# Kernel optimization log

Hardware: AMD Instinct MI355X
Metric: run time of the kernel (lower is better)

## Reference

```python
import jax, jax.numpy as jnp
import numpy as np

B, F_DIM, T = 16, 256, 4096
L = 128           # latent_dim
CF = 2            # combineVQ_frames
K = 2             # codebook_num
M = 1024          # codebook_size (n_embeddings)
D = L * CF // K   # codebook_dim = 128
TC = T // CF      # combined frames
ALPHA = -5.0      # distance->logit scale
TAU = 2.0         # max_temp (curr_temp at init)


def setup_inputs() -> dict:
    key = jax.random.key(0)
    k1, k2, k3, k4, k5 = jax.random.split(key, 5)
    inputs = jax.random.normal(k1, (B, F_DIM, T, 1), dtype=jnp.float32)
    # xavier-ish scaled 1x1 conv weights
    w1 = jax.random.normal(k2, (L, F_DIM), dtype=jnp.float32) * (2.0 / (L + F_DIM)) ** 0.5
    w2 = jax.random.normal(k3, (F_DIM, L), dtype=jnp.float32) * (2.0 / (L + F_DIM)) ** 0.5
    # codebooks init uniform(-1, 1) as in nn.init.uniform_(a=-1, b=1)
    codebooks = jax.random.uniform(k4, (K, M, D), dtype=jnp.float32, minval=-1.0, maxval=1.0)
    # gumbel noise that torch's F.gumbel_softmax would sample internally
    u = jax.random.uniform(k5, (K, B * TC, M), dtype=jnp.float32, minval=1e-7, maxval=1.0 - 1e-7)
    gumbels = -jnp.log(-jnp.log(u))
    return {"inputs": inputs, "w1": w1, "w2": w2, "codebooks": codebooks, "gumbels": gumbels}


def _vq_layer(vq_in, emb, g):
    # vq_in: [B, TC, D], emb: [M, D], g: [B*TC, M]
    xf = vq_in.reshape(-1, D)  # [N, D]
    dist = (jnp.sum(emb ** 2, axis=1)[None, :]
            + jnp.sum(xf ** 2, axis=1, keepdims=True)
            - 2.0 * (xf @ emb.T))                      # [N, M]
    logits = ALPHA * dist
    # straight-through hard gumbel-softmax (training path of F.gumbel_softmax(hard=True))
    y_soft = jax.nn.softmax((logits + g) / TAU, axis=-1)
    idx = jnp.argmax(y_soft, axis=-1)                  # [N]
    y_hard = jax.nn.one_hot(idx, M, dtype=y_soft.dtype)
    y = y_hard + y_soft - jax.lax.stop_gradient(y_soft)
    q = y @ emb                                        # [N, D] dequantize
    return q.reshape(B, TC, D), idx.reshape(B, TC)


def reference(inputs, w1, w2, codebooks, gumbels):
    # conv1x1_1: [B, F, T, 1] -> [B, L, T, 1]; then squeeze(-1).permute(0,2,1) -> [B, T, L]
    x = jnp.einsum('bfto,lf->btl', inputs, w1)         # [B, T, L]
    # combine frames and split channels across codebooks
    xc = x.reshape(B, TC, CF, L)                       # [B, TC, CF, L]
    chunks = jnp.split(xc, K, axis=-1)                 # K x [B, TC, CF, L/K]
    quants, inds = [], []
    for i in range(K):
        vq_in = chunks[i].reshape(B, TC, D)            # CF*(L/K) == D
        q, idx = _vq_layer(vq_in, codebooks[i], gumbels[i])
        quants.append(q.reshape(B, TC, CF, L // K))
        inds.append(idx)
    vq_feat = jnp.concatenate(quants, axis=-1).reshape(B, T, L)  # [B, T, L]
    # conv1x1_2: back to [B, F, T, 1]
    out = jnp.einsum('btl,fl->bft', vq_feat, w2)[..., None]
    quant_inds = jnp.stack(inds, axis=-1)              # [B, TC, K]
    return out, vq_feat, quant_inds
```

## Files before the change

kernel.cpp:

```cpp
#include <hip/hip_runtime.h>
#include <cstdint>
#include <cmath>

#define B_ 16
#define F_ 256
#define T_ 4096
#define L_ 128
#define TC_ 2048
#define D_ 128
#define M_ 1024
#define NROWS_ 32768

#define PAD 132

__global__ __launch_bounds__(256) void gemm1_kernel(
    const float* __restrict__ in, const float* __restrict__ w1,
    float* __restrict__ x) {
  __shared__ float As[32 * PAD];
  __shared__ float Bs[32 * PAD];
  const int tid = threadIdx.x;
  const int blk = blockIdx.x;
  const int b = blk >> 5;
  const int t0 = (blk & 31) << 7;
  const int tm = tid & 15;
  const int tr = tid >> 4;
  const float* inb = in + (size_t)b * F_ * T_;
  float acc[8][8];
#pragma unroll
  for (int i = 0; i < 8; ++i)
#pragma unroll
    for (int j = 0; j < 8; ++j) acc[i][j] = 0.f;

  for (int f0 = 0; f0 < F_; f0 += 32) {
#pragma unroll
    for (int it = 0; it < 4; ++it) {
      int e = tid + it * 256;
      int ff = e >> 5, q = e & 31;
      float4 v = *(const float4*)(inb + (size_t)(f0 + ff) * T_ + t0 + q * 4);
      *(float4*)(&As[ff * PAD + q * 4]) = v;
    }
#pragma unroll
    for (int it = 0; it < 4; ++it) {
      int e = tid + it * 256;
      int l = e >> 3, q = e & 7;
      float4 v = *(const float4*)(w1 + l * F_ + f0 + q * 4);
      Bs[(q * 4 + 0) * PAD + l] = v.x;
      Bs[(q * 4 + 1) * PAD + l] = v.y;
      Bs[(q * 4 + 2) * PAD + l] = v.z;
      Bs[(q * 4 + 3) * PAD + l] = v.w;
    }
    __syncthreads();
#pragma unroll
    for (int ff = 0; ff < 32; ++ff) {
      float a[8], w[8];
      *(float4*)&a[0] = *(const float4*)&As[ff * PAD + tr * 8];
      *(float4*)&a[4] = *(const float4*)&As[ff * PAD + tr * 8 + 4];
      *(float4*)&w[0] = *(const float4*)&Bs[ff * PAD + tm * 8];
      *(float4*)&w[4] = *(const float4*)&Bs[ff * PAD + tm * 8 + 4];
#pragma unroll
      for (int i = 0; i < 8; ++i)
#pragma unroll
        for (int j = 0; j < 8; ++j) acc[i][j] = fmaf(a[i], w[j], acc[i][j]);
    }
    __syncthreads();
  }
  float* xb = x + ((size_t)b * T_ + t0) * L_;
#pragma unroll
  for (int i = 0; i < 8; ++i) {
    float* dst = xb + (size_t)(tr * 8 + i) * L_ + tm * 8;
    *(float4*)(dst) = make_float4(acc[i][0], acc[i][1], acc[i][2], acc[i][3]);
    *(float4*)(dst + 4) = make_float4(acc[i][4], acc[i][5], acc[i][6], acc[i][7]);
  }
}

__global__ __launch_bounds__(256) void c2_kernel(const float* __restrict__ cbs,
                                                 float* __restrict__ c2) {
  int m = blockIdx.x * 256 + threadIdx.x;
  const float* row = cbs + (size_t)m * D_;
  float s = 0.f;
#pragma unroll
  for (int d = 0; d < D_; d += 4) {
    float4 v = *(const float4*)(row + d);
    s += v.x * v.x;
    s += v.y * v.y;
    s += v.z * v.z;
    s += v.w * v.w;
  }
  c2[m] = s;
}

__global__ __launch_bounds__(256) void vq_kernel(
    const float* __restrict__ x, const float* __restrict__ cbs,
    const float* __restrict__ gum, const float* __restrict__ c2,
    float* __restrict__ vq_feat, float* __restrict__ qinds) {
  __shared__ float smem[2 * 32 * PAD];
  __shared__ int widx[128];
  float* Xs = smem;
  float* Es = smem + 32 * PAD;
  const int tid = threadIdx.x;
  const int blk = blockIdx.x;
  const int cb = blk >> 8;
  const int n0 = (blk & 255) << 7;
  const int tm = tid & 15;
  const int tr = tid >> 4;
  const float* cbp = cbs + (size_t)cb * M_ * D_;
  const float* gp = gum + (size_t)cb * NROWS_ * M_;
  const float* c2p = c2 + cb * M_;

  float best[8];
  int bidx[8];
#pragma unroll
  for (int i = 0; i < 8; ++i) {
    best[i] = -INFINITY;
    bidx[i] = 0;
  }

  for (int mt = 0; mt < 8; ++mt) {
    const int m0 = mt << 7;
    float acc[8][8];
#pragma unroll
    for (int i = 0; i < 8; ++i)
#pragma unroll
      for (int j = 0; j < 8; ++j) acc[i][j] = 0.f;

    for (int d0 = 0; d0 < D_; d0 += 32) {
      const int cf = d0 >> 6;
      const int j0 = d0 & 63;
#pragma unroll
      for (int it = 0; it < 4; ++it) {
        int e = tid + it * 256;
        int r = e >> 3, q = e & 7;
        int n = n0 + r;
        int bb = n >> 11, tc = n & 2047;
        const float* src =
            x + ((size_t)bb * T_ + 2 * tc + cf) * L_ + cb * 64 + j0 + q * 4;
        float4 v = *(const float4*)src;
        Xs[(q * 4 + 0) * PAD + r] = v.x;
        Xs[(q * 4 + 1) * PAD + r] = v.y;
        Xs[(q * 4 + 2) * PAD + r] = v.z;
        Xs[(q * 4 + 3) * PAD + r] = v.w;
      }
#pragma unroll
      for (int it = 0; it < 4; ++it) {
        int e = tid + it * 256;
        int mm = e >> 3, q = e & 7;
        const float* src = cbp + (size_t)(m0 + mm) * D_ + d0 + q * 4;
        float4 v = *(const float4*)src;
        Es[(q * 4 + 0) * PAD + mm] = v.x;
        Es[(q * 4 + 1) * PAD + mm] = v.y;
        Es[(q * 4 + 2) * PAD + mm] = v.z;
        Es[(q * 4 + 3) * PAD + mm] = v.w;
      }
      __syncthreads();
#pragma unroll
      for (int dd = 0; dd < 32; ++dd) {
        float a[8], w[8];
        *(float4*)&a[0] = *(const float4*)&Xs[dd * PAD + tr * 8];
        *(float4*)&a[4] = *(const float4*)&Xs[dd * PAD + tr * 8 + 4];
        *(float4*)&w[0] = *(const float4*)&Es[dd * PAD + tm * 8];
        *(float4*)&w[4] = *(const float4*)&Es[dd * PAD + tm * 8 + 4];
#pragma unroll
        for (int i = 0; i < 8; ++i)
#pragma unroll
          for (int j = 0; j < 8; ++j) acc[i][j] = fmaf(a[i], w[j], acc[i][j]);
      }
      __syncthreads();
    }
    float cc[8];
    *(float4*)&cc[0] = *(const float4*)(c2p + m0 + tm * 8);
    *(float4*)&cc[4] = *(const float4*)(c2p + m0 + tm * 8 + 4);
#pragma unroll
    for (int i = 0; i < 8; ++i) {
      int n = n0 + tr * 8 + i;
      const float* grow = gp + (size_t)n * M_ + m0 + tm * 8;
      float g[8];
      *(float4*)&g[0] = *(const float4*)grow;
      *(float4*)&g[4] = *(const float4*)(grow + 4);
#pragma unroll
      for (int j = 0; j < 8; ++j) {
        float dist = cc[j] - 2.f * acc[i][j];
        float sc = fmaf(-5.f, dist, g[j]);
        if (sc > best[i]) {
          best[i] = sc;
          bidx[i] = m0 + tm * 8 + j;
        }
      }
    }
  }
  float* rbest = smem;
  int* ridx = (int*)(smem + 128 * 17);
#pragma unroll
  for (int i = 0; i < 8; ++i) {
    rbest[(tr * 8 + i) * 17 + tm] = best[i];
    ridx[(tr * 8 + i) * 17 + tm] = bidx[i];
  }
  __syncthreads();
  if (tid < 128) {
    float bv = rbest[tid * 17];
    int bi = ridx[tid * 17];
#pragma unroll
    for (int k = 1; k < 16; ++k) {
      float v = rbest[tid * 17 + k];
      int ii = ridx[tid * 17 + k];
      if (v > bv || (v == bv && ii < bi)) {
        bv = v;
        bi = ii;
      }
    }
    widx[tid] = bi;
    int n = n0 + tid;
    qinds[(size_t)n * 2 + cb] = (float)bi;
  }
  __syncthreads();
  const int jj = (tid & 15) * 4;
  for (int seg = tid >> 4; seg < 256; seg += 16) {
    int r = seg >> 1, cf = seg & 1;
    int wi = widx[r];
    float4 v = *(const float4*)(cbp + (size_t)wi * D_ + cf * 64 + jj);
    int n = n0 + r;
    int bb = n >> 11, tc = n & 2047;
    float* dst = vq_feat + ((size_t)bb * T_ + 2 * tc + cf) * L_ + cb * 64 + jj;
    *(float4*)dst = v;
  }
}

__global__ __launch_bounds__(256) void gemm2_kernel(
    const float* __restrict__ vq, const float* __restrict__ w2,
    float* __restrict__ out) {
  __shared__ float As[32 * PAD];
  __shared__ float Bs[32 * PAD];
  const int tid = threadIdx.x;
  const int blk = blockIdx.x;
  const int b = blk >> 6;
  const int rest = blk & 63;
  const int t0 = (rest >> 1) << 7;
  const int f0 = (rest & 1) << 7;
  const int tm = tid & 15;
  const int tr = tid >> 4;
  const float* vb = vq + (size_t)b * T_ * L_;
  float acc[8][8];
#pragma unroll
  for (int i = 0; i < 8; ++i)
#pragma unroll
    for (int j = 0; j < 8; ++j) acc[i][j] = 0.f;

  for (int l0 = 0; l0 < L_; l0 += 32) {
#pragma unroll
    for (int it = 0; it < 4; ++it) {
      int e = tid + it * 256;
      int t = e >> 3, q = e & 7;
      float4 v = *(const float4*)(vb + (size_t)(t0 + t) * L_ + l0 + q * 4);
      As[(q * 4 + 0) * PAD + t] = v.x;
      As[(q * 4 + 1) * PAD + t] = v.y;
      As[(q * 4 + 2) * PAD + t] = v.z;
      As[(q * 4 + 3) * PAD + t] = v.w;
    }
#pragma unroll
    for (int it = 0; it < 4; ++it) {
      int e = tid + it * 256;
      int f = e >> 3, q = e & 7;
      float4 v = *(const float4*)(w2 + (size_t)(f0 + f) * L_ + l0 + q * 4);
      Bs[(q * 4 + 0) * PAD + f] = v.x;
      Bs[(q * 4 + 1) * PAD + f] = v.y;
      Bs[(q * 4 + 2) * PAD + f] = v.z;
      Bs[(q * 4 + 3) * PAD + f] = v.w;
    }
    __syncthreads();
#pragma unroll
    for (int dd = 0; dd < 32; ++dd) {
      float a[8], w[8];
      *(float4*)&a[0] = *(const float4*)&As[dd * PAD + tr * 8];
      *(float4*)&a[4] = *(const float4*)&As[dd * PAD + tr * 8 + 4];
      *(float4*)&w[0] = *(const float4*)&Bs[dd * PAD + tm * 8];
      *(float4*)&w[4] = *(const float4*)&Bs[dd * PAD + tm * 8 + 4];
#pragma unroll
      for (int i = 0; i < 8; ++i)
#pragma unroll
        for (int j = 0; j < 8; ++j) acc[i][j] = fmaf(a[i], w[j], acc[i][j]);
    }
    __syncthreads();
  }
  float* ob = out + ((size_t)b * F_ + f0) * T_ + t0;
#pragma unroll
  for (int j = 0; j < 8; ++j) {
    float* dst = ob + (size_t)(tm * 8 + j) * T_ + tr * 8;
    *(float4*)dst = make_float4(acc[0][j], acc[1][j], acc[2][j], acc[3][j]);
    *(float4*)(dst + 4) = make_float4(acc[4][j], acc[5][j], acc[6][j], acc[7][j]);
  }
}

extern "C" void kernel_launch(void* const* d_in, const int* in_sizes, int n_in,
                              void* d_out, int out_size, void* d_ws,
                              size_t ws_size, hipStream_t stream) {
  const float* in = (const float*)d_in[0];
  const float* w1 = (const float*)d_in[1];
  const float* w2 = (const float*)d_in[2];
  const float* cbs = (const float*)d_in[3];
  const float* gum = (const float*)d_in[4];
  float* out = (float*)d_out;
  float* vq_feat = out + 16777216;
  float* qinds = out + 25165824;
  float* x = out;
  float* c2 = out + 8388608;

  hipLaunchKernelGGL(gemm1_kernel, dim3(512), dim3(256), 0, stream, in, w1, x);
  hipLaunchKernelGGL(c2_kernel, dim3(8), dim3(256), 0, stream, cbs, c2);
  hipLaunchKernelGGL(vq_kernel, dim3(512), dim3(256), 0, stream, x, cbs, gum,
                     c2, vq_feat, qinds);
  hipLaunchKernelGGL(gemm2_kernel, dim3(1024), dim3(256), 0, stream, vq_feat,
                     w2, out);
}
```

Before: 674.7 us.

## Halve per-block tile to 64x128 with split column mapping across all GEMM kernels

```diff
diff --git a/kernel.cpp b/kernel.cpp
--- a/kernel.cpp
+++ b/kernel.cpp
@@ -11,54 +11,56 @@
 #define M_ 1024
 #define NROWS_ 32768
 
-#define PAD 132
+#define PA 68
+#define PB 132
 
 __global__ __launch_bounds__(256) void gemm1_kernel(
     const float* __restrict__ in, const float* __restrict__ w1,
     float* __restrict__ x) {
-  __shared__ float As[32 * PAD];
-  __shared__ float Bs[32 * PAD];
+  __shared__ float As[32 * PA];
+  __shared__ float Bs[32 * PB];
   const int tid = threadIdx.x;
   const int blk = blockIdx.x;
-  const int b = blk >> 5;
-  const int t0 = (blk & 31) << 7;
+  const int b = blk >> 6;
+  const int t0 = (blk & 63) << 6;
   const int tm = tid & 15;
   const int tr = tid >> 4;
   const float* inb = in + (size_t)b * F_ * T_;
-  float acc[8][8];
-#pragma unroll
-  for (int i = 0; i < 8; ++i)
+  float acc[4][8];
+#pragma unroll
+  for (int i = 0; i < 4; ++i)
 #pragma unroll
     for (int j = 0; j < 8; ++j) acc[i][j] = 0.f;
 
   for (int f0 = 0; f0 < F_; f0 += 32) {
+#pragma unroll
+    for (int it = 0; it < 2; ++it) {
+      int e = tid + it * 256;
+      int ff = e >> 4, tq = e & 15;
+      float4 v = *(const float4*)(inb + (size_t)(f0 + ff) * T_ + t0 + tq * 4);
+      *(float4*)(&As[ff * PA + tq * 4]) = v;
+    }
 #pragma unroll
     for (int it = 0; it < 4; ++it) {
       int e = tid + it * 256;
-      int ff = e >> 5, q = e & 31;
-      float4 v = *(const float4*)(inb + (size_t)(f0 + ff) * T_ + t0 + q * 4);
-      *(float4*)(&As[ff * PAD + q * 4]) = v;
-    }
-#pragma unroll
-    for (int it = 0; it < 4; ++it) {
-      int e = tid + it * 256;
-      int l = e >> 3, q = e & 7;
+      int llow = e & 15, rest = e >> 4;
+      int q = rest & 7, lhigh = rest >> 3;
+      int l = lhigh * 16 + llow;
       float4 v = *(const float4*)(w1 + l * F_ + f0 + q * 4);
-      Bs[(q * 4 + 0) * PAD + l] = v.x;
-      Bs[(q * 4 + 1) * PAD + l] = v.y;
-      Bs[(q * 4 + 2) * PAD + l] = v.z;
-      Bs[(q * 4 + 3) * PAD + l] = v.w;
+      Bs[(q * 4 + 0) * PB + l] = v.x;
+      Bs[(q * 4 + 1) * PB + l] = v.y;
+      Bs[(q * 4 + 2) * PB + l] = v.z;
+      Bs[(q * 4 + 3) * PB + l] = v.w;
     }
     __syncthreads();
 #pragma unroll
     for (int ff = 0; ff < 32; ++ff) {
-      float a[8], w[8];
-      *(float4*)&a[0] = *(const float4*)&As[ff * PAD + tr * 8];
-      *(float4*)&a[4] = *(const float4*)&As[ff * PAD + tr * 8 + 4];
-      *(float4*)&w[0] = *(const float4*)&Bs[ff * PAD + tm * 8];
-      *(float4*)&w[4] = *(const float4*)&Bs[ff * PAD + tm * 8 + 4];
-#pragma unroll
-      for (int i = 0; i < 8; ++i)
+      float a[4], w[8];
+      *(float4*)&a[0] = *(const float4*)&As[ff * PA + tr * 4];
+      *(float4*)&w[0] = *(const float4*)&Bs[ff * PB + tm * 4];
+      *(float4*)&w[4] = *(const float4*)&Bs[ff * PB + 64 + tm * 4];
+#pragma unroll
+      for (int i = 0; i < 4; ++i)
 #pragma unroll
         for (int j = 0; j < 8; ++j) acc[i][j] = fmaf(a[i], w[j], acc[i][j]);
     }
@@ -66,10 +68,10 @@
   }
   float* xb = x + ((size_t)b * T_ + t0) * L_;
 #pragma unroll
-  for (int i = 0; i < 8; ++i) {
-    float* dst = xb + (size_t)(tr * 8 + i) * L_ + tm * 8;
+  for (int i = 0; i < 4; ++i) {
+    float* dst = xb + (size_t)(tr * 4 + i) * L_ + tm * 4;
     *(float4*)(dst) = make_float4(acc[i][0], acc[i][1], acc[i][2], acc[i][3]);
-    *(float4*)(dst + 4) = make_float4(acc[i][4], acc[i][5], acc[i][6], acc[i][7]);
+    *(float4*)(dst + 64) = make_float4(acc[i][4], acc[i][5], acc[i][6], acc[i][7]);
   }
 }
 
@@ -93,33 +95,33 @@
     const float* __restrict__ x, const float* __restrict__ cbs,
     const float* __restrict__ gum, const float* __restrict__ c2,
     float* __restrict__ vq_feat, float* __restrict__ qinds) {
-  __shared__ float smem[2 * 32 * PAD];
-  __shared__ int widx[128];
+  __shared__ float smem[32 * PA + 32 * PB];
+  __shared__ int widx[64];
   float* Xs = smem;
-  float* Es = smem + 32 * PAD;
+  float* Es = smem + 32 * PA;
   const int tid = threadIdx.x;
   const int blk = blockIdx.x;
-  const int cb = blk >> 8;
-  const int n0 = (blk & 255) << 7;
+  const int cb = blk >> 9;
+  const int n0 = (blk & 511) << 6;
   const int tm = tid & 15;
   const int tr = tid >> 4;
   const float* cbp = cbs + (size_t)cb * M_ * D_;
   const float* gp = gum + (size_t)cb * NROWS_ * M_;
   const float* c2p = c2 + cb * M_;
 
-  float best[8];
-  int bidx[8];
-#pragma unroll
-  for (int i = 0; i < 8; ++i) {
+  float best[4];
+  int bidx[4];
+#pragma unroll
+  for (int i = 0; i < 4; ++i) {
     best[i] = -INFINITY;
     bidx[i] = 0;
   }
 
   for (int mt = 0; mt < 8; ++mt) {
     const int m0 = mt << 7;
-    float acc[8][8];
-#pragma unroll
-    for (int i = 0; i < 8; ++i)
+    float acc[4][8];
+#pragma unroll
+    for (int i = 0; i < 4; ++i)
 #pragma unroll
       for (int j = 0; j < 8; ++j) acc[i][j] = 0.f;
 
@@ -127,75 +129,79 @@
       const int cf = d0 >> 6;
       const int j0 = d0 & 63;
 #pragma unroll
-      for (int it = 0; it < 4; ++it) {
+      for (int it = 0; it < 2; ++it) {
         int e = tid + it * 256;
-        int r = e >> 3, q = e & 7;
+        int rlow = e & 15, rest = e >> 4;
+        int q = rest & 7, rhigh = rest >> 3;
+        int r = rhigh * 16 + rlow;
         int n = n0 + r;
         int bb = n >> 11, tc = n & 2047;
         const float* src =
             x + ((size_t)bb * T_ + 2 * tc + cf) * L_ + cb * 64 + j0 + q * 4;
         float4 v = *(const float4*)src;
-        Xs[(q * 4 + 0) * PAD + r] = v.x;
-        Xs[(q * 4 + 1) * PAD + r] = v.y;
-        Xs[(q * 4 + 2) * PAD + r] = v.z;
-        Xs[(q * 4 + 3) * PAD + r] = v.w;
+        Xs[(q * 4 + 0) * PA + r] = v.x;
+        Xs[(q * 4 + 1) * PA + r] = v.y;
+        Xs[(q * 4 + 2) * PA + r] = v.z;
+        Xs[(q * 4 + 3) * PA + r] = v.w;
       }
 #pragma unroll
       for (int it = 0; it < 4; ++it) {
         int e = tid + it * 256;
-        int mm = e >> 3, q = e & 7;
+        int mlow = e & 15, rest = e >> 4;
+        int q = rest & 7, mhigh = rest >> 3;
+        int mm = mhigh * 16 + mlow;
         const float* src = cbp + (size_t)(m0 + mm) * D_ + d0 + q * 4;
         float4 v = *(const float4*)src;
-        Es[(q * 4 + 0) * PAD + mm] = v.x;
-        Es[(q * 4 + 1) * PAD + mm] = v.y;
-        Es[(q * 4 + 2) * PAD + mm] = v.z;
-        Es[(q * 4 + 3) * PAD + mm] = v.w;
+        Es[(q * 4 + 0) * PB + mm] = v.x;
+        Es[(q * 4 + 1) * PB + mm] = v.y;
+        Es[(q * 4 + 2) * PB + mm] = v.z;
+        Es[(q * 4 + 3) * PB + mm] = v.w;
       }
       __syncthreads();
 #pragma unroll
       for (int dd = 0; dd < 32; ++dd) {
-        float a[8], w[8];
-        *(float4*)&a[0] = *(const float4*)&Xs[dd * PAD + tr * 8];
-        *(float4*)&a[4] = *(const float4*)&Xs[dd * PAD + tr * 8 + 4];
-        *(float4*)&w[0] = *(const float4*)&Es[dd * PAD + tm * 8];
-        *(float4*)&w[4] = *(const float4*)&Es[dd * PAD + tm * 8 + 4];
-#pragma unroll
-        for (int i = 0; i < 8; ++i)
+        float a[4], w[8];
+        *(float4*)&a[0] = *(const float4*)&Xs[dd * PA + tr * 4];
+        *(float4*)&w[0] = *(const float4*)&Es[dd * PB + tm * 4];
+        *(float4*)&w[4] = *(const float4*)&Es[dd * PB + 64 + tm * 4];
+#pragma unroll
+        for (int i = 0; i < 4; ++i)
 #pragma unroll
           for (int j = 0; j < 8; ++j) acc[i][j] = fmaf(a[i], w[j], acc[i][j]);
       }
       __syncthreads();
     }
     float cc[8];
-    *(float4*)&cc[0] = *(const float4*)(c2p + m0 + tm * 8);
-    *(float4*)&cc[4] = *(const float4*)(c2p + m0 + tm * 8 + 4);
-#pragma unroll
-    for (int i = 0; i < 8; ++i) {
-      int n = n0 + tr * 8 + i;
-      const float* grow = gp + (size_t)n * M_ + m0 + tm * 8;
+    *(float4*)&cc[0] = *(const float4*)(c2p + m0 + tm * 4);
+    *(float4*)&cc[4] = *(const float4*)(c2p + m0 + 64 + tm * 4);
+#pragma unroll
+    for (int i = 0; i < 4; ++i) {
+      int n = n0 + tr * 4 + i;
+      const float* grow = gp + (size_t)n * M_ + m0 + tm * 4;
       float g[8];
       *(float4*)&g[0] = *(const float4*)grow;
-      *(float4*)&g[4] = *(const float4*)(grow + 4);
+      *(float4*)&g[4] = *(const float4*)(grow + 64);
 #pragma unroll
       for (int j = 0; j < 8; ++j) {
         float dist = cc[j] - 2.f * acc[i][j];
         float sc = fmaf(-5.f, dist, g[j]);
+        int m = (j < 4) ? (m0 + tm * 4 + j) : (m0 + 64 + tm * 4 + j - 4);
         if (sc > best[i]) {
           best[i] = sc;
-          bidx[i] = m0 + tm * 8 + j;
+          bidx[i] = m;
         }
       }
     }
   }
   float* rbest = smem;
-  int* ridx = (int*)(smem + 128 * 17);
-#pragma unroll
-  for (int i = 0; i < 8; ++i) {
-    rbest[(tr * 8 + i) * 17 + tm] = best[i];
-    ridx[(tr * 8 + i) * 17 + tm] = bidx[i];
+  int* ridx = (int*)(smem + 64 * 17);
+#pragma unroll
+  for (int i = 0; i < 4; ++i) {
+    rbest[(tr * 4 + i) * 17 + tm] = best[i];
+    ridx[(tr * 4 + i) * 17 + tm] = bidx[i];
   }
   __syncthreads();
-  if (tid < 128) {
+  if (tid < 64) {
     float bv = rbest[tid * 17];
     int bi = ridx[tid * 17];
 #pragma unroll
@@ -212,14 +218,17 @@
     qinds[(size_t)n * 2 + cb] = (float)bi;
   }
   __syncthreads();
-  const int jj = (tid & 15) * 4;
-  for (int seg = tid >> 4; seg < 256; seg += 16) {
-    int r = seg >> 1, cf = seg & 1;
+#pragma unroll
+  for (int it = 0; it < 8; ++it) {
+    int e = tid + it * 256;
+    int r = e >> 5, qd = e & 31;
     int wi = widx[r];
-    float4 v = *(const float4*)(cbp + (size_t)wi * D_ + cf * 64 + jj);
+    float4 v = *(const float4*)(cbp + (size_t)wi * D_ + qd * 4);
+    int cf = qd >> 4;
     int n = n0 + r;
     int bb = n >> 11, tc = n & 2047;
-    float* dst = vq_feat + ((size_t)bb * T_ + 2 * tc + cf) * L_ + cb * 64 + jj;
+    float* dst =
+        vq_feat + ((size_t)bb * T_ + 2 * tc + cf) * L_ + cb * 64 + (qd & 15) * 4;
     *(float4*)dst = v;
   }
 }
@@ -227,54 +236,56 @@
 __global__ __launch_bounds__(256) void gemm2_kernel(
     const float* __restrict__ vq, const float* __restrict__ w2,
     float* __restrict__ out) {
-  __shared__ float As[32 * PAD];
-  __shared__ float Bs[32 * PAD];
+  __shared__ float Ws[32 * PA];
+  __shared__ float Vs[32 * PB];
   const int tid = threadIdx.x;
   const int blk = blockIdx.x;
-  const int b = blk >> 6;
-  const int rest = blk & 63;
-  const int t0 = (rest >> 1) << 7;
-  const int f0 = (rest & 1) << 7;
+  const int b = blk >> 7;
+  const int f0 = ((blk >> 5) & 3) << 6;
+  const int t0 = (blk & 31) << 7;
   const int tm = tid & 15;
   const int tr = tid >> 4;
   const float* vb = vq + (size_t)b * T_ * L_;
-  float acc[8][8];
-#pragma unroll
-  for (int i = 0; i < 8; ++i)
+  float acc[4][8];
+#pragma unroll
+  for (int i = 0; i < 4; ++i)
 #pragma unroll
     for (int j = 0; j < 8; ++j) acc[i][j] = 0.f;
 
   for (int l0 = 0; l0 < L_; l0 += 32) {
+#pragma unroll
+    for (int it = 0; it < 2; ++it) {
+      int e = tid + it * 256;
+      int flow = e & 15, rest = e >> 4;
+      int q = rest & 7, fhigh = rest >> 3;
+      int f = fhigh * 16 + flow;
+      float4 v = *(const float4*)(w2 + (size_t)(f0 + f) * L_ + l0 + q * 4);
+      Ws[(q * 4 + 0) * PA + f] = v.x;
+      Ws[(q * 4 + 1) * PA + f] = v.y;
+      Ws[(q * 4 + 2) * PA + f] = v.z;
+      Ws[(q * 4 + 3) * PA + f] = v.w;
+    }
 #pragma unroll
     for (int it = 0; it < 4; ++it) {
       int e = tid + it * 256;
-      int t = e >> 3, q = e & 7;
+      int tlow = e & 15, rest = e >> 4;
+      int q = rest & 7, thigh = rest >> 3;
+      int t = thigh * 16 + tlow;
       float4 v = *(const float4*)(vb + (size_t)(t0 + t) * L_ + l0 + q * 4);
-      As[(q * 4 + 0) * PAD + t] = v.x;
-      As[(q * 4 + 1) * PAD + t] = v.y;
-      As[(q * 4 + 2) * PAD + t] = v.z;
-      As[(q * 4 + 3) * PAD + t] = v.w;
-    }
-#pragma unroll
-    for (int it = 0; it < 4; ++it) {
-      int e = tid + it * 256;
-      int f = e >> 3, q = e & 7;
-      float4 v = *(const float4*)(w2 + (size_t)(f0 + f) * L_ + l0 + q * 4);
-      Bs[(q * 4 + 0) * PAD + f] = v.x;
-      Bs[(q * 4 + 1) * PAD + f] = v.y;
-      Bs[(q * 4 + 2) * PAD + f] = v.z;
-      Bs[(q * 4 + 3) * PAD + f] = v.w;
+      Vs[(q * 4 + 0) * PB + t] = v.x;
+      Vs[(q * 4 + 1) * PB + t] = v.y;
+      Vs[(q * 4 + 2) * PB + t] = v.z;
+      Vs[(q * 4 + 3) * PB + t] = v.w;
     }
     __syncthreads();
 #pragma unroll
-    for (int dd = 0; dd < 32; ++dd) {
-      float a[8], w[8];
-      *(float4*)&a[0] = *(const float4*)&As[dd * PAD + tr * 8];
-      *(float4*)&a[4] = *(const float4*)&As[dd * PAD + tr * 8 + 4];
-      *(float4*)&w[0] = *(const float4*)&Bs[dd * PAD + tm * 8];
-      *(float4*)&w[4] = *(const float4*)&Bs[dd * PAD + tm * 8 + 4];
-#pragma unroll
-      for (int i = 0; i < 8; ++i)
+    for (int ll = 0; ll < 32; ++ll) {
+      float a[4], w[8];
+      *(float4*)&a[0] = *(const float4*)&Ws[ll * PA + tr * 4];
+      *(float4*)&w[0] = *(const float4*)&Vs[ll * PB + tm * 4];
+      *(float4*)&w[4] = *(const float4*)&Vs[ll * PB + 64 + tm * 4];
+#pragma unroll
+      for (int i = 0; i < 4; ++i)
 #pragma unroll
         for (int j = 0; j < 8; ++j) acc[i][j] = fmaf(a[i], w[j], acc[i][j]);
     }
@@ -282,10 +293,10 @@
   }
   float* ob = out + ((size_t)b * F_ + f0) * T_ + t0;
 #pragma unroll
-  for (int j = 0; j < 8; ++j) {
-    float* dst = ob + (size_t)(tm * 8 + j) * T_ + tr * 8;
-    *(float4*)dst = make_float4(acc[0][j], acc[1][j], acc[2][j], acc[3][j]);
-    *(float4*)(dst + 4) = make_float4(acc[4][j], acc[5][j], acc[6][j], acc[7][j]);
+  for (int i = 0; i < 4; ++i) {
+    float* dst = ob + (size_t)(tr * 4 + i) * T_ + tm * 4;
+    *(float4*)dst = make_float4(acc[i][0], acc[i][1], acc[i][2], acc[i][3]);
+    *(float4*)(dst + 64) = make_float4(acc[i][4], acc[i][5], acc[i][6], acc[i][7]);
   }
 }
 
@@ -303,10 +314,10 @@
   float* x = out;
   float* c2 = out + 8388608;
 
-  hipLaunchKernelGGL(gemm1_kernel, dim3(512), dim3(256), 0, stream, in, w1, x);
+  hipLaunchKernelGGL(gemm1_kernel, dim3(1024), dim3(256), 0, stream, in, w1, x);
   hipLaunchKernelGGL(c2_kernel, dim3(8), dim3(256), 0, stream, cbs, c2);
-  hipLaunchKernelGGL(vq_kernel, dim3(512), dim3(256), 0, stream, x, cbs, gum,
+  hipLaunchKernelGGL(vq_kernel, dim3(1024), dim3(256), 0, stream, x, cbs, gum,
                      c2, vq_feat, qinds);
-  hipLaunchKernelGGL(gemm2_kernel, dim3(1024), dim3(256), 0, stream, vq_feat,
+  hipLaunchKernelGGL(gemm2_kernel, dim3(2048), dim3(256), 0, stream, vq_feat,
                      w2, out);
 }
```

Measured after the change: 681.2 us. Within noise of the previous version (+1.0%).
